# Kernel tuning notes

Hardware: AMD Instinct MI355X
Metric: run time of the kernel (lower is better)

## Reference

```python
import jax, jax.numpy as jnp
import numpy as np


def setup_inputs() -> dict:
    key = jax.random.key(0)
    k1, k2 = jax.random.split(key)
    B, C, H, W = 8, 64, 128, 512
    image_tensor = jax.random.normal(k1, (B, C, H, W), dtype=jnp.float32)
    # positive metric depths in ~[1, 56] m
    depth = jax.random.uniform(k2, (B, H, W), dtype=jnp.float32) * 55.0 + 1.0
    fx = fy = 500.0; cx = 512.0; cy = 128.0  # intrinsics for original 1024x256 image
    camera_k = jnp.tile(jnp.array([[fx, 0.0, cx], [0.0, fy, cy], [0.0, 0.0, 1.0]],
                                  dtype=jnp.float32)[None], (B, 1, 1))
    meter_per_pixel = jnp.full((1,), 0.25, dtype=jnp.float32)
    return {"image_tensor": image_tensor, "camera_k": camera_k, "depth": depth,
            "meter_per_pixel": meter_per_pixel, "sat_width": 512,
            "ori_grdH": 256, "ori_grdW": 1024}


def reference(image_tensor, camera_k, depth, meter_per_pixel, sat_width, ori_grdH, ori_grdW):
    B, C, H, W = image_tensor.shape
    half = sat_width // 2
    mpp = meter_per_pixel.reshape(())

    # scale intrinsics from original image size to feature-map size (rows 0 and 1)
    row_scale = jnp.array([W / ori_grdW, H / ori_grdH, 1.0], dtype=jnp.float32)
    ck = camera_k * row_scale[None, :, None]
    k_inv = jnp.linalg.inv(ck)  # [B,3,3]

    # back-project pixel grid: xyz_w[b,h,w,:] = K^-1 @ [u,v,1]
    v, u = jnp.meshgrid(jnp.arange(H, dtype=jnp.float32),
                        jnp.arange(W, dtype=jnp.float32), indexing='ij')
    uv1 = jnp.stack([u, v, jnp.ones_like(u)], axis=-1)          # [H,W,3]
    xyz_w = jnp.einsum('bij,hwj->bhwi', k_inv, uv1)             # [B,H,W,3]
    # depth is already at (H,W): bilinear same-size resize is identity
    xyz = (xyz_w * depth[..., None] * 1.2).reshape(B * H * W, 3)

    feats = image_tensor.transpose(0, 2, 3, 1).reshape(B * H * W, C)

    # voxelize x,z (torch .long() truncates toward zero)
    x = jnp.trunc(xyz[:, 0] / mpp).astype(jnp.int32)
    z = jnp.trunc(xyz[:, 2] / mpp).astype(jnp.int32)
    y = xyz[:, 1]
    b = jnp.repeat(jnp.arange(B, dtype=jnp.int32), H * W)

    kept = (x >= -half) & (x <= half - 1) & (z >= -half) & (z <= half - 1)
    max_h = jnp.max(jnp.where(kept, y, -jnp.inf))
    xx = x + half
    zz = z + half
    h = max_h - y  # height key; the last entry per voxel (max h) survives dedup

    # voxel rank (same encoding as torch); out-of-bounds points get a sentinel
    rank0 = zz * (sat_width * B) + (xx + 1) * B + b
    SENT = sat_width * sat_width * B + B
    rank0 = jnp.where(kept, rank0, SENT)

    # torch: sort by h, then stable sort by rank0  == lexsort(primary=rank0, secondary=h)
    order = jnp.lexsort((h, rank0))
    r_s = rank0[order]
    f_s = feats[order]
    b_s, xx_s, zz_s = b[order], xx[order], zz[order]

    # keep the last point of each rank0 group (highest h in that voxel)
    is_last = jnp.concatenate([r_s[:-1] != r_s[1:], jnp.array([True])])
    valid = is_last & (r_s != SENT)

    flat = b_s * (sat_width * sat_width) + xx_s * sat_width + zz_s
    flat = jnp.where(valid, flat, B * sat_width * sat_width)  # invalid -> OOB, dropped

    final = jnp.zeros((B * sat_width * sat_width, C), dtype=jnp.float32)
    final = final.at[flat].set(f_s, mode='drop')
    return final.reshape(B, sat_width, sat_width, C).transpose(0, 3, 1, 2)
```

## Files before the change

### kernel.cpp

```cpp
#include <hip/hip_runtime.h>

#define BB 8
#define CC 64
#define HH 128
#define WW 512
#define SS 512
#define HALF 256
#define HWP (HH * WW)
#define BHW (BB * HWP)
#define CELLS (BB * SS * SS)
#define NSHARD 8

__device__ __forceinline__ unsigned int order_f32(float f) {
    unsigned int u = __float_as_uint(f);
    return (u & 0x80000000u) ? ~u : (u | 0x80000000u);
}

__global__ __launch_bounds__(256) void proj_kernel(
    const float* __restrict__ img,
    const float* __restrict__ camera_k,
    const float* __restrict__ depth,
    const float* __restrict__ mpp_p,
    unsigned long long* __restrict__ keys8,
    float* __restrict__ img_t)
{
    __shared__ float sk[9];
    __shared__ float tile[64][65];

    const int gp0 = blockIdx.x * 256;
    const int b   = gp0 >> 16;
    const int t   = threadIdx.x;
    const int idx = gp0 + t;

    if (t == 0) {
        const float rs[3] = {0.5f, 0.5f, 1.0f};
        double a[9];
        #pragma unroll
        for (int i = 0; i < 3; ++i)
            #pragma unroll
            for (int j = 0; j < 3; ++j)
                a[i*3 + j] = (double)__fmul_rn(camera_k[b*9 + i*3 + j], rs[i]);
        double det = a[0]*(a[4]*a[8]-a[5]*a[7])
                   - a[1]*(a[3]*a[8]-a[5]*a[6])
                   + a[2]*(a[3]*a[7]-a[4]*a[6]);
        double inv[9];
        inv[0] =  (a[4]*a[8]-a[5]*a[7])/det;
        inv[1] = -(a[1]*a[8]-a[2]*a[7])/det;
        inv[2] =  (a[1]*a[5]-a[2]*a[4])/det;
        inv[3] = -(a[3]*a[8]-a[5]*a[6])/det;
        inv[4] =  (a[0]*a[8]-a[2]*a[6])/det;
        inv[5] = -(a[0]*a[5]-a[2]*a[3])/det;
        inv[6] =  (a[3]*a[7]-a[4]*a[6])/det;
        inv[7] = -(a[0]*a[7]-a[1]*a[6])/det;
        inv[8] =  (a[0]*a[4]-a[1]*a[3])/det;
        #pragma unroll
        for (int i = 0; i < 9; ++i) sk[i] = (float)inv[i];
    }
    __syncthreads();

    {
        const int rem = idx & (HWP - 1);
        const int v = rem >> 9;
        const int u = rem & (WW - 1);
        const float d = depth[idx];
        const float mpp = mpp_p[0];
        const float uf = (float)u, vf = (float)v;

        float xw = __fadd_rn(__fadd_rn(__fmul_rn(sk[0], uf), __fmul_rn(sk[1], vf)), sk[2]);
        float yw = __fadd_rn(__fadd_rn(__fmul_rn(sk[3], uf), __fmul_rn(sk[4], vf)), sk[5]);
        float zw = __fadd_rn(__fadd_rn(__fmul_rn(sk[6], uf), __fmul_rn(sk[7], vf)), sk[8]);
        float x3 = __fmul_rn(__fmul_rn(xw, d), 1.2f);
        float y3 = __fmul_rn(__fmul_rn(yw, d), 1.2f);
        float z3 = __fmul_rn(__fmul_rn(zw, d), 1.2f);

        int xi = (int)truncf(__fdiv_rn(x3, mpp));
        int zi = (int)truncf(__fdiv_rn(z3, mpp));

        if (xi >= -HALF && xi <= HALF - 1 && zi >= -HALF && zi <= HALF - 1) {
            int cell = (b << 18) | ((xi + HALF) << 9) | (zi + HALF);
            unsigned long long key =
                ((unsigned long long)order_f32(y3) << 32) | (unsigned int)(~idx);
            unsigned int xcc;
            asm volatile("s_getreg_b32 %0, hwreg(HW_REG_XCC_ID)" : "=s"(xcc));
            unsigned long long* shard = keys8 + (size_t)(xcc & (NSHARD - 1)) * CELLS;
            __hip_atomic_fetch_min(&shard[cell], key,
                                   __ATOMIC_RELAXED, __HIP_MEMORY_SCOPE_WORKGROUP);
        }
    }

    const int lane = t & 63;
    const int grp  = t >> 6;
    const int p0   = gp0 & (HWP - 1);
    const float* src = img + (size_t)b * CC * HWP + p0;
    float*       dst = img_t + (size_t)gp0 * CC;

    #pragma unroll
    for (int s4 = 0; s4 < 4; ++s4) {
        __syncthreads();
        const float* ssrc = src + s4 * 64;
        #pragma unroll
        for (int i = 0; i < 16; ++i) {
            int ch = grp * 16 + i;
            tile[lane][ch] = ssrc[(size_t)ch * HWP + lane];
        }
        __syncthreads();
        float* sdst = dst + (size_t)(s4 * 64) * CC;
        #pragma unroll
        for (int i = 0; i < 16; ++i) {
            int p = grp * 16 + i;
            sdst[(size_t)p * CC + lane] = tile[p][lane];
        }
    }
}

__global__ __launch_bounds__(256) void scatter_kernel(
    const float* __restrict__ img_t,
    const unsigned long long* __restrict__ keys8,
    float* __restrict__ out)
{
    __shared__ float sT[128 * 64];
    __shared__ int   sRem[128];

    const int cell0 = blockIdx.x * 128;
    const int b     = cell0 >> 18;
    const int t     = threadIdx.x;
    const int w     = t >> 6;
    const int l     = t & 63;

    if (t < 128) {
        const unsigned long long* kp = keys8 + cell0 + t;
        unsigned long long k = ~0ull;
        #pragma unroll
        for (int s = 0; s < NSHARD; ++s) {
            unsigned long long ks = kp[(size_t)s * CELLS];
            k = ks < k ? ks : k;
        }
        sRem[t] = (k == ~0ull) ? -1
                : (int)((~(unsigned int)(k & 0xFFFFFFFFull)) & (HWP - 1));
    }
    __syncthreads();

    const size_t bHWP = (size_t)b * HWP;
    #pragma unroll 8
    for (int i = 0; i < 32; ++i) {
        int cell = w * 32 + i;
        int r = sRem[cell];
        float val = 0.0f;
        if (r >= 0)
            val = img_t[((bHWP + (size_t)r) << 6) + l];
        sT[(cell << 6) + (l ^ (cell & 31))] = val;
    }
    __syncthreads();

    const int local = cell0 & (SS * SS - 1);
    float* op = out + (size_t)b * CC * (SS * SS) + local;
    #pragma unroll
    for (int j = 0; j < 16; ++j) {
        int c = w * 16 + j;
        float v0 = sT[((l)      << 6) + (c ^ (l & 31))];
        float v1 = sT[((l + 64) << 6) + (c ^ (l & 31))];
        float* oc = op + (size_t)c * (SS * SS);
        oc[l]      = v0;
        oc[64 + l] = v1;
    }
}

extern "C" void kernel_launch(void* const* d_in, const int* in_sizes, int n_in,
                              void* d_out, int out_size, void* d_ws, size_t ws_size,
                              hipStream_t stream) {
    const float* img      = (const float*)d_in[0];
    const float* camera_k = (const float*)d_in[1];
    const float* depth    = (const float*)d_in[2];
    const float* mpp      = (const float*)d_in[3];

    unsigned long long* keys8 = (unsigned long long*)d_ws;
    float* img_t = (float*)((char*)d_ws + ((size_t)128 << 20));

    hipMemsetAsync(keys8, 0xFF, (size_t)NSHARD * CELLS * sizeof(unsigned long long), stream);

    proj_kernel<<<BHW / 256, 256, 0, stream>>>(img, camera_k, depth, mpp, keys8, img_t);
    scatter_kernel<<<CELLS / 128, 256, 0, stream>>>(img_t, keys8, (float*)d_out);
}
```

Baseline: 854.5 us.

## Drop per-XCC key shards and rewrite scatter without shared-memory transpose

Replaces the eight per-XCC shards of voxel keys with a single device-wide atomicMin array. This cuts the memset and the eight-way key reduction in the scatter pass, at the cost of cross-XCC atomic contention. The scatter kernel now handles 16 cells per wave. It broadcasts each cell's source row with a shuffle, reads channels directly into registers, and writes the output with nontemporal stores instead of staging through a shared-memory transpose. Empty waves skip the gather entirely.

```diff
diff --git a/kernel.cpp b/kernel.cpp
--- a/kernel.cpp
+++ b/kernel.cpp
@@ -8,8 +8,8 @@
 #define HALF 256
 #define HWP (HH * WW)
 #define BHW (BB * HWP)
+#define SSSS (SS * SS)
 #define CELLS (BB * SS * SS)
-#define NSHARD 8
 
 __device__ __forceinline__ unsigned int order_f32(float f) {
     unsigned int u = __float_as_uint(f);
@@ -21,7 +21,7 @@
     const float* __restrict__ camera_k,
     const float* __restrict__ depth,
     const float* __restrict__ mpp_p,
-    unsigned long long* __restrict__ keys8,
+    unsigned long long* __restrict__ keys,
     float* __restrict__ img_t)
 {
     __shared__ float sk[9];
@@ -80,11 +80,7 @@
             int cell = (b << 18) | ((xi + HALF) << 9) | (zi + HALF);
             unsigned long long key =
                 ((unsigned long long)order_f32(y3) << 32) | (unsigned int)(~idx);
-            unsigned int xcc;
-            asm volatile("s_getreg_b32 %0, hwreg(HW_REG_XCC_ID)" : "=s"(xcc));
-            unsigned long long* shard = keys8 + (size_t)(xcc & (NSHARD - 1)) * CELLS;
-            __hip_atomic_fetch_min(&shard[cell], key,
-                                   __ATOMIC_RELAXED, __HIP_MEMORY_SCOPE_WORKGROUP);
+            atomicMin(&keys[cell], key);
         }
     }
 
@@ -115,53 +111,44 @@
 
 __global__ __launch_bounds__(256) void scatter_kernel(
     const float* __restrict__ img_t,
-    const unsigned long long* __restrict__ keys8,
+    const unsigned long long* __restrict__ keys,
     float* __restrict__ out)
 {
-    __shared__ float sT[128 * 64];
-    __shared__ int   sRem[128];
-
-    const int cell0 = blockIdx.x * 128;
+    const int cell0 = blockIdx.x * 64;
     const int b     = cell0 >> 18;
     const int t     = threadIdx.x;
     const int w     = t >> 6;
     const int l     = t & 63;
+    const int zc    = l & 15;
+    const int csub  = l >> 4;
+    const int cbase = cell0 + w * 16;
 
-    if (t < 128) {
-        const unsigned long long* kp = keys8 + cell0 + t;
-        unsigned long long k = ~0ull;
+    int myrem = -1;
+    if (l < 16) {
+        unsigned long long k = keys[cbase + l];
+        myrem = (k == ~0ull) ? -1
+              : (int)((~(unsigned int)(k & 0xFFFFFFFFull)) & (HWP - 1));
+    }
+    const int rem = __shfl(myrem, zc);
+
+    float v[16];
+    if (__any(rem >= 0)) {
+        const float* rec = img_t +
+            (((size_t)b * HWP + (size_t)(rem >= 0 ? rem : 0)) << 6);
         #pragma unroll
-        for (int s = 0; s < NSHARD; ++s) {
-            unsigned long long ks = kp[(size_t)s * CELLS];
-            k = ks < k ? ks : k;
-        }
-        sRem[t] = (k == ~0ull) ? -1
-                : (int)((~(unsigned int)(k & 0xFFFFFFFFull)) & (HWP - 1));
+        for (int k = 0; k < 16; ++k)
+            v[k] = (rem >= 0) ? rec[4 * k + csub] : 0.0f;
+    } else {
+        #pragma unroll
+        for (int k = 0; k < 16; ++k) v[k] = 0.0f;
     }
-    __syncthreads();
 
-    const size_t bHWP = (size_t)b * HWP;
-    #pragma unroll 8
-    for (int i = 0; i < 32; ++i) {
-        int cell = w * 32 + i;
-        int r = sRem[cell];
-        float val = 0.0f;
-        if (r >= 0)
-            val = img_t[((bHWP + (size_t)r) << 6) + l];
-        sT[(cell << 6) + (l ^ (cell & 31))] = val;
-    }
-    __syncthreads();
-
-    const int local = cell0 & (SS * SS - 1);
-    float* op = out + (size_t)b * CC * (SS * SS) + local;
+    const int localw = cbase & (SSSS - 1);
+    float* op = out + (size_t)b * CC * SSSS + localw + zc;
     #pragma unroll
-    for (int j = 0; j < 16; ++j) {
-        int c = w * 16 + j;
-        float v0 = sT[((l)      << 6) + (c ^ (l & 31))];
-        float v1 = sT[((l + 64) << 6) + (c ^ (l & 31))];
-        float* oc = op + (size_t)c * (SS * SS);
-        oc[l]      = v0;
-        oc[64 + l] = v1;
+    for (int k = 0; k < 16; ++k) {
+        int c = 4 * k + csub;
+        __builtin_nontemporal_store(v[k], op + (size_t)c * SSSS);
     }
 }
 
@@ -173,11 +160,11 @@
     const float* depth    = (const float*)d_in[2];
     const float* mpp      = (const float*)d_in[3];
 
-    unsigned long long* keys8 = (unsigned long long*)d_ws;
-    float* img_t = (float*)((char*)d_ws + ((size_t)128 << 20));
+    unsigned long long* keys = (unsigned long long*)d_ws;
+    float* img_t = (float*)((char*)d_ws + ((size_t)32 << 20));
 
-    hipMemsetAsync(keys8, 0xFF, (size_t)NSHARD * CELLS * sizeof(unsigned long long), stream);
+    hipMemsetAsync(keys, 0xFF, (size_t)CELLS * sizeof(unsigned long long), stream);
 
-    proj_kernel<<<BHW / 256, 256, 0, stream>>>(img, camera_k, depth, mpp, keys8, img_t);
-    scatter_kernel<<<CELLS / 128, 256, 0, stream>>>(img_t, keys8, (float*)d_out);
+    proj_kernel<<<BHW / 256, 256, 0, stream>>>(img, camera_k, depth, mpp, keys, img_t);
+    scatter_kernel<<<CELLS / 64, 256, 0, stream>>>(img_t, keys, (float*)d_out);
 }
```

After: 812.5 us. -4.9%, faster.
